# Optimization experiments

Hardware: AMD Instinct MI355X
Metric: run time of the kernel (lower is better)

## Reference

```python
import jax, jax.numpy as jnp
import numpy as np

SEF = 64   # skipped edge features (MLPGraphNetwork default sef)
SNF = 64   # skipped node features (MLPGraphNetwork default snf)
NR_STEPS = 3


def mlp2(x, W0, b0, W1, b1):
    # MyMLP with multI=1.0, relu hidden, linear last, no layernorm
    return jax.nn.relu(x @ W0 + b0) @ W1 + b1


def setup_inputs() -> dict:
    N, E = 50000, 800000
    nrNodeF, nrEdgeF, nrEmbed, nrTypes = 32, 3, 16, 2
    key = jax.random.key(0)
    ks = jax.random.split(key, 20)

    def w(k, fi, fo):
        # torch.normal(0,1) * (2.0 / fan_in)  (relu init in MyMLP)
        return jax.random.normal(k, (fi, fo), jnp.float32) * (2.0 / fi)

    z = lambda n: jnp.zeros((n,), jnp.float32)
    return {
        "edge_index": jax.random.randint(ks[0], (2, E), 0, N),
        "nodeFeatures": jax.random.uniform(ks[1], (N, nrNodeF), jnp.float32),
        "edgeFeatures": jax.random.normal(ks[2], (E, nrEdgeF), jnp.float32),
        "emb": jax.random.normal(ks[3], (nrTypes, nrEmbed), jnp.float32),
        "enc_n_W0": w(ks[4], nrNodeF - 1 + nrEmbed, 128), "enc_n_b0": z(128),
        "enc_n_W1": w(ks[5], 128, 128), "enc_n_b1": z(128),
        "enc_e_W0": w(ks[6], nrEdgeF, 128), "enc_e_b0": z(128),
        "enc_e_W1": w(ks[7], 128, 128), "enc_e_b1": z(128),
        "core_e_W0": w(ks[8], 192, 128), "core_e_b0": z(128),
        "core_e_W1": w(ks[9], 128, 64), "core_e_b1": z(64),
        "core_n_W0": w(ks[10], 128, 128), "core_n_b0": z(128),
        "core_n_W1": w(ks[11], 128, 64), "core_n_b1": z(64),
        "dec_W0": w(ks[12], 128, 128), "dec_b0": z(128),
        "dec_W1": w(ks[13], 128, 3), "dec_b1": z(3),
    }


def reference(edge_index, nodeFeatures, edgeFeatures, emb,
              enc_n_W0, enc_n_b0, enc_n_W1, enc_n_b1,
              enc_e_W0, enc_e_b0, enc_e_W1, enc_e_b1,
              core_e_W0, core_e_b0, core_e_W1, core_e_b1,
              core_n_W0, core_n_b0, core_n_W1, core_n_b1,
              dec_W0, dec_b0, dec_W1, dec_b1):
    N = nodeFeatures.shape[0]
    src, dst = edge_index[0], edge_index[1]  # j (source), i (target)

    # encode: embed particle type from last node feature column
    ptype = (nodeFeatures[:, -1] + 0.5).astype(jnp.int32)
    node = jnp.concatenate([nodeFeatures[:, :-1], emb[ptype]], axis=-1)
    node = mlp2(node, enc_n_W0, enc_n_b0, enc_n_W1, enc_n_b1)          # [N,128]
    edge = mlp2(edgeFeatures, enc_e_W0, enc_e_b0, enc_e_W1, enc_e_b1)  # [E,128]

    ones = jnp.ones((edge_index.shape[1],), node.dtype)
    counts = jnp.maximum(jax.ops.segment_sum(ones, dst, num_segments=N), 1.0)

    # process: shared MLPGraphNetwork applied NR_STEPS times
    for _ in range(NR_STEPS):
        einp = jnp.concatenate([edge[:, SEF:], node[dst][:, SNF:], node[src][:, SNF:]], axis=-1)  # [E,192]
        eout = mlp2(einp, core_e_W0, core_e_b0, core_e_W1, core_e_b1)  # [E,64]
        edge = jnp.concatenate([edge[:, :SEF], edge[:, SEF:] + eout], axis=-1)  # residual tail, [E,128]
        agg = jax.ops.segment_sum(edge, dst, num_segments=N) / counts[:, None]  # mean aggr, [N,128]
        ninp = jnp.concatenate([agg[:, SEF:], node[:, SNF:]], axis=-1)  # [N,128]
        nout = mlp2(ninp, core_n_W0, core_n_b0, core_n_W1, core_n_b1)  # [N,64]
        node = jnp.concatenate([node[:, :SNF], node[:, SNF:] + nout], axis=-1)  # [N,128]

    # decode
    return mlp2(node, dec_W0, dec_b0, dec_W1, dec_b1)  # [N,3]
```

## Files before the change

kernel.cpp:

```cpp
#include <hip/hip_runtime.h>
#include <cstdint>
#include <cstddef>


__global__ void k_zero(int* __restrict__ p, int n) {
    int i = blockIdx.x * 256 + threadIdx.x;
    if (i < n) p[i] = 0;
}


__global__ void k_hist(const int* __restrict__ dst, int* __restrict__ counts, int E) {
    int e = blockIdx.x * 256 + threadIdx.x;
    if (e < E) atomicAdd(&counts[dst[e]], 1);
}

__global__ __launch_bounds__(1024) void k_scan(
    const int* __restrict__ counts, int* __restrict__ row_off,
    int* __restrict__ cursor, float* __restrict__ inv_cnt, int N) {
    __shared__ int wsum[16];
    int t = threadIdx.x;
    int wave = t >> 6, lane = t & 63;
    int carry = 0;
    for (int base = 0; base < N; base += 1024) {
        int i = base + t;
        int v = (i < N) ? counts[i] : 0;
        int s = v;
        #pragma unroll
        for (int off = 1; off < 64; off <<= 1) {
            int u = __shfl_up(s, off, 64);
            if (lane >= off) s += u;
        }
        if (lane == 63) wsum[wave] = s;
        __syncthreads();
        int wpre = 0, full = 0;
        #pragma unroll
        for (int wv = 0; wv < 16; wv++) {
            int x = wsum[wv];
            full += x;
            if (wv < wave) wpre += x;
        }
        if (i < N) {
            int excl = carry + wpre + s - v;
            row_off[i] = excl;
            cursor[i]  = excl;
            inv_cnt[i] = 1.0f / (float)((v > 0) ? v : 1);
        }
        carry += full;
        __syncthreads();
    }
    if (t == 0) row_off[N] = carry;
}

__global__ void k_fill(const int* __restrict__ dst, int* __restrict__ cursor,
                       int* __restrict__ edge_list, int E) {
    int e = blockIdx.x * 256 + threadIdx.x;
    if (e < E) {
        int pos = atomicAdd(&cursor[dst[e]], 1);
        edge_list[pos] = e;
    }
}

__global__ void k_perm_idx(const int* __restrict__ elist,
                           const int* __restrict__ src, const int* __restrict__ dst,
                           int* __restrict__ src_p, int* __restrict__ dst_p, int E) {
    int i = blockIdx.x * 256 + threadIdx.x;
    if (i < E) {
        int e = elist[i];
        src_p[i] = src[e];
        dst_p[i] = dst[e];
    }
}


__global__ void k_embW(const float* __restrict__ emb, const float* __restrict__ W0,
                       const float* __restrict__ b0, float* __restrict__ embW) {
    int c = threadIdx.x;
    #pragma unroll
    for (int p = 0; p < 2; p++) {
        float acc = b0[c];
        #pragma unroll
        for (int k = 0; k < 16; k++)
            acc = fmaf(emb[p * 16 + k], W0[(31 + k) * 128 + c], acc);
        embW[p * 128 + c] = acc;
    }
}


__device__ __forceinline__ void g1_accum32(
    const float4* __restrict__ a4, int kk4,
    const float* __restrict__ W, int cbase, float* __restrict__ h) {
    #pragma clang loop unroll(disable)
    for (int kk = 0; kk < kk4; kk++) {
        float4 a = a4[kk];
        const float* wr = W + (size_t)kk * 4 * 128 + cbase;
        const float4* w0 = reinterpret_cast<const float4*>(wr);
        const float4* w1 = reinterpret_cast<const float4*>(wr + 128);
        const float4* w2 = reinterpret_cast<const float4*>(wr + 256);
        const float4* w3 = reinterpret_cast<const float4*>(wr + 384);
        #pragma unroll
        for (int cg = 0; cg < 8; cg++) {
            float4 p = w0[cg], q = w1[cg], r = w2[cg], s = w3[cg];
            h[cg*4+0] = fmaf(a.w, s.x, fmaf(a.z, r.x, fmaf(a.y, q.x, fmaf(a.x, p.x, h[cg*4+0]))));
            h[cg*4+1] = fmaf(a.w, s.y, fmaf(a.z, r.y, fmaf(a.y, q.y, fmaf(a.x, p.y, h[cg*4+1]))));
            h[cg*4+2] = fmaf(a.w, s.z, fmaf(a.z, r.z, fmaf(a.y, q.z, fmaf(a.x, p.z, h[cg*4+2]))));
            h[cg*4+3] = fmaf(a.w, s.w, fmaf(a.z, r.w, fmaf(a.y, q.w, fmaf(a.x, p.w, h[cg*4+3]))));
        }
    }
}

__device__ __forceinline__ void g1_tail3(
    float x, float y, float z, const float* __restrict__ W, int cbase,
    float* __restrict__ h) {
    const float4* w0 = reinterpret_cast<const float4*>(W + cbase);
    const float4* w1 = reinterpret_cast<const float4*>(W + 128 + cbase);
    const float4* w2 = reinterpret_cast<const float4*>(W + 256 + cbase);
    #pragma unroll
    for (int cg = 0; cg < 8; cg++) {
        float4 p = w0[cg], q = w1[cg], r = w2[cg];
        h[cg*4+0] = fmaf(z, r.x, fmaf(y, q.x, fmaf(x, p.x, h[cg*4+0])));
        h[cg*4+1] = fmaf(z, r.y, fmaf(y, q.y, fmaf(x, p.y, h[cg*4+1])));
        h[cg*4+2] = fmaf(z, r.z, fmaf(y, q.z, fmaf(x, p.z, h[cg*4+2])));
        h[cg*4+3] = fmaf(z, r.w, fmaf(y, q.w, fmaf(x, p.w, h[cg*4+3])));
    }
}

__device__ __forceinline__ void g2_accum64(
    float* __restrict__ sb, const float* __restrict__ hc,
    const float* __restrict__ W1, int kbase, int rs, float* __restrict__ o) {
    int t = threadIdx.x;
    #pragma unroll
    for (int k = 0; k < 32; k++) sb[k * 256 + t] = hc[k];
    __syncthreads();
    #pragma clang loop unroll(disable)
    for (int k = 0; k < 32; k++) {
        float hk = sb[k * 256 + t];
        const float4* w = reinterpret_cast<const float4*>(W1 + (size_t)(kbase + k) * rs);
        #pragma unroll
        for (int cg = 0; cg < 16; cg++) {
            float4 wv = w[cg];
            o[cg*4+0] = fmaf(hk, wv.x, o[cg*4+0]);
            o[cg*4+1] = fmaf(hk, wv.y, o[cg*4+1]);
            o[cg*4+2] = fmaf(hk, wv.z, o[cg*4+2]);
            o[cg*4+3] = fmaf(hk, wv.w, o[cg*4+3]);
        }
    }
    __syncthreads();
}


__global__ __launch_bounds__(256, 2) void k_enc_node_tail(
    const float* __restrict__ nodeF, const float* __restrict__ embW,
    const float* __restrict__ W0, const float* __restrict__ W1,
    const float* __restrict__ b1, float* __restrict__ nodeT, int N) {
    __shared__ float sb[32 * 256];
    int n = blockIdx.x * 256 + threadIdx.x;
    bool valid = n < N;
    int nc = valid ? n : N - 1;
    const float4* nf4 = reinterpret_cast<const float4*>(nodeF + (size_t)nc * 32);
    float4 v7 = nf4[7];
    int p = (int)(v7.w + 0.5f);
    const float4* ew = reinterpret_cast<const float4*>(embW + p * 128);

    float o[64];
    const float4* bv = reinterpret_cast<const float4*>(b1 + 64);
    #pragma unroll
    for (int i = 0; i < 16; i++) {
        float4 b = bv[i];
        o[4*i+0] = b.x; o[4*i+1] = b.y; o[4*i+2] = b.z; o[4*i+3] = b.w;
    }
    #pragma unroll
    for (int ch = 0; ch < 4; ch++) {
        int cbase = ch * 32;
        float h[32];
        #pragma unroll
        for (int i = 0; i < 8; i++) {
            float4 u = ew[ch*8 + i];
            h[4*i+0] = u.x; h[4*i+1] = u.y; h[4*i+2] = u.z; h[4*i+3] = u.w;
        }
        g1_accum32(nf4, 7, W0, cbase, h);
        g1_tail3(v7.x, v7.y, v7.z, W0 + 28*128, cbase, h);
        #pragma unroll
        for (int i = 0; i < 32; i++) h[i] = fmaxf(h[i], 0.0f);
        g2_accum64(sb, h, W1 + 64, cbase, 128, o);
    }
    if (valid) {
        float4* out4 = reinterpret_cast<float4*>(nodeT + (size_t)n * 64);
        #pragma unroll
        for (int i = 0; i < 16; i++)
            out4[i] = make_float4(o[4*i], o[4*i+1], o[4*i+2], o[4*i+3]);
    }
}


__global__ __launch_bounds__(256, 3) void k_enc_edge_T(
    const float* __restrict__ edgeF, const int* __restrict__ perm, int usePerm,
    const float* __restrict__ W0, const float* __restrict__ b0,
    const float* __restrict__ W1, const float* __restrict__ b1,
    float* __restrict__ edgeT, int E) {
    __shared__ float H[128 * 65];
    __shared__ float Wbuf[32 * 68];
    __shared__ float Xs[64 * 4];

    int t = threadIdx.x;
    int base = blockIdx.x * 64;

    if (t < 192) {
        int i = t / 3, j = t - i * 3;
        int e = base + i; int ec = (e < E) ? e : E - 1;
        int e2 = usePerm ? perm[ec] : ec;
        Xs[i * 4 + j] = edgeF[(size_t)e2 * 3 + j];
    }
    __syncthreads();

    int eg = t & 15, cg = t >> 4;
    float c1[4][8];
    {
        float4 b0a = *reinterpret_cast<const float4*>(b0 + cg * 8);
        float4 b0b = *reinterpret_cast<const float4*>(b0 + cg * 8 + 4);
        float bb[8] = {b0a.x,b0a.y,b0a.z,b0a.w,b0b.x,b0b.y,b0b.z,b0b.w};
        #pragma unroll
        for (int ie = 0; ie < 4; ie++)
            #pragma unroll
            for (int jc = 0; jc < 8; jc++) c1[ie][jc] = bb[jc];
    }
    #pragma unroll
    for (int k = 0; k < 3; k++) {
        float4 wa = *reinterpret_cast<const float4*>(W0 + k * 128 + cg * 8);
        float4 wb = *reinterpret_cast<const float4*>(W0 + k * 128 + cg * 8 + 4);
        float ww[8] = {wa.x,wa.y,wa.z,wa.w,wb.x,wb.y,wb.z,wb.w};
        #pragma unroll
        for (int ie = 0; ie < 4; ie++) {
            float a = Xs[(eg + 16 * ie) * 4 + k];
            #pragma unroll
            for (int jc = 0; jc < 8; jc++)
                c1[ie][jc] = fmaf(a, ww[jc], c1[ie][jc]);
        }
    }

    int wr_r = t >> 3, wr_cb = t & 7;
    float4 wreg2[2];
    {
        const float4* wr = reinterpret_cast<const float4*>(
            W1 + (size_t)(wr_r) * 128 + 64 + wr_cb * 8);
        wreg2[0] = wr[0]; wreg2[1] = wr[1];
    }

    #pragma unroll
    for (int ie = 0; ie < 4; ie++)
        #pragma unroll
        for (int jc = 0; jc < 8; jc++)
            H[(cg * 8 + jc) * 65 + eg + 16 * ie] = fmaxf(c1[ie][jc], 0.0f);

    int eg2 = t & 15, cg2 = t >> 4;
    float c2[4][4];
    {
        float4 bv = *reinterpret_cast<const float4*>(b1 + 64 + cg2 * 4);
        #pragma unroll
        for (int ie = 0; ie < 4; ie++) {
            c2[ie][0]=bv.x; c2[ie][1]=bv.y; c2[ie][2]=bv.z; c2[ie][3]=bv.w;
        }
    }
    #pragma clang loop unroll(disable)
    for (int phase = 0; phase < 4; phase++) {
        __syncthreads();
        {
            float* wd = Wbuf + wr_r * 68 + wr_cb * 8;
            wd[0]=wreg2[0].x; wd[1]=wreg2[0].y; wd[2]=wreg2[0].z; wd[3]=wreg2[0].w;
            wd[4]=wreg2[1].x; wd[5]=wreg2[1].y; wd[6]=wreg2[1].z; wd[7]=wreg2[1].w;
        }
        __syncthreads();
        if (phase < 3) {
            const float4* wr = reinterpret_cast<const float4*>(
                W1 + (size_t)((phase + 1) * 32 + wr_r) * 128 + 64 + wr_cb * 8);
            wreg2[0] = wr[0]; wreg2[1] = wr[1];
        }
        #pragma clang loop unroll_count(4)
        for (int k = 0; k < 32; k++) {
            int c = phase * 32 + k;
            float a0 = H[c*65 + eg2*4 + 0];
            float a1 = H[c*65 + eg2*4 + 1];
            float a2 = H[c*65 + eg2*4 + 2];
            float a3 = H[c*65 + eg2*4 + 3];
            float4 b4 = *reinterpret_cast<const float4*>(Wbuf + k * 68 + cg2 * 4);
            float bb[4] = {b4.x, b4.y, b4.z, b4.w};
            #pragma unroll
            for (int jc = 0; jc < 4; jc++) {
                c2[0][jc] = fmaf(a0, bb[jc], c2[0][jc]);
                c2[1][jc] = fmaf(a1, bb[jc], c2[1][jc]);
                c2[2][jc] = fmaf(a2, bb[jc], c2[2][jc]);
                c2[3][jc] = fmaf(a3, bb[jc], c2[3][jc]);
            }
        }
    }
    #pragma unroll
    for (int ie = 0; ie < 4; ie++) {
        int e = base + eg2 * 4 + ie;
        if (e < E) {
            *reinterpret_cast<float4*>(edgeT + (size_t)e * 64 + cg2 * 4) =
                make_float4(c2[ie][0], c2[ie][1], c2[ie][2], c2[ie][3]);
        }
    }
}


__global__ __launch_bounds__(256, 4) void k_node_pre_d(
    const float* __restrict__ nodeT, const float* __restrict__ W0,
    const float* __restrict__ b0, float* __restrict__ Pd, int N) {
    int n = blockIdx.x * 256 + threadIdx.x;
    bool valid = n < N;
    int nc = valid ? n : N - 1;
    const float4* a4 = reinterpret_cast<const float4*>(nodeT + (size_t)nc * 64);

    #pragma unroll
    for (int ch = 0; ch < 4; ch++) {
        int cbase = ch * 32;
        float h[32];
        const float4* b0v = reinterpret_cast<const float4*>(b0 + cbase);
        #pragma unroll
        for (int i = 0; i < 8; i++) {
            float4 b = b0v[i];
            h[4*i+0] = b.x; h[4*i+1] = b.y; h[4*i+2] = b.z; h[4*i+3] = b.w;
        }
        g1_accum32(a4, 16, W0 + 64*128, cbase, h);
        if (valid) {
            float4* o4 = reinterpret_cast<float4*>(Pd + (size_t)n * 128 + cbase);
            #pragma unroll
            for (int i = 0; i < 8; i++)
                o4[i] = make_float4(h[4*i], h[4*i+1], h[4*i+2], h[4*i+3]);
        }
    }
}


__global__ __launch_bounds__(256, 3) void k_edge_core_T(
    float* __restrict__ edgeT, const float* __restrict__ Pd,
    const float* __restrict__ nodeT,
    const int* __restrict__ srcI, const int* __restrict__ dstI,
    const float* __restrict__ W0, const float* __restrict__ W1,
    const float* __restrict__ b1, int E) {
    __shared__ float Abuf[2 * 64 * 65];
    __shared__ float Wbuf[32 * 132];

    int t = threadIdx.x;
    int base = blockIdx.x * 64;

    {
        int i = t >> 2, q = t & 3;
        int e = base + i; int ec = (e < E) ? e : E - 1;
        const float4* er = reinterpret_cast<const float4*>(edgeT + (size_t)ec * 64 + q * 16);
        int s = srcI[ec];
        const float4* sr = reinterpret_cast<const float4*>(nodeT + (size_t)s * 64 + q * 16);
        float* ae = Abuf + i * 65 + q * 16;
        float* as = Abuf + 64 * 65 + i * 65 + q * 16;
        #pragma unroll
        for (int j4 = 0; j4 < 4; j4++) {
            float4 v = er[j4];
            ae[j4*4+0]=v.x; ae[j4*4+1]=v.y; ae[j4*4+2]=v.z; ae[j4*4+3]=v.w;
            float4 w = sr[j4];
            as[j4*4+0]=w.x; as[j4*4+1]=w.y; as[j4*4+2]=w.z; as[j4*4+3]=w.w;
        }
    }

    int eg = t & 15, cg = t >> 4;
    float c1[4][8];
    #pragma unroll
    for (int ie = 0; ie < 4; ie++) {
        int e = base + eg + 16 * ie; int ec = (e < E) ? e : E - 1;
        int d = dstI[ec];
        const float4* pr = reinterpret_cast<const float4*>(Pd + (size_t)d * 128 + cg * 8);
        float4 p0 = pr[0], p1 = pr[1];
        c1[ie][0]=p0.x; c1[ie][1]=p0.y; c1[ie][2]=p0.z; c1[ie][3]=p0.w;
        c1[ie][4]=p1.x; c1[ie][5]=p1.y; c1[ie][6]=p1.z; c1[ie][7]=p1.w;
    }

    int wr_r = t >> 3, wr_cb = t & 7;
    float4 wreg[4];
    {
        const float4* wr = reinterpret_cast<const float4*>(
            W0 + (size_t)(0 + wr_r) * 128 + wr_cb * 16);
        wreg[0]=wr[0]; wreg[1]=wr[1]; wreg[2]=wr[2]; wreg[3]=wr[3];
    }
    #pragma clang loop unroll(disable)
    for (int phase = 0; phase < 4; phase++) {
        const float* Asrc = Abuf + ((phase < 2) ? 0 : 64 * 65);
        int koff = (phase & 1) * 32;
        __syncthreads();
        {
            float* wd = Wbuf + wr_r * 132 + wr_cb * 16;
            #pragma unroll
            for (int j4 = 0; j4 < 4; j4++) {
                wd[j4*4+0]=wreg[j4].x; wd[j4*4+1]=wreg[j4].y;
                wd[j4*4+2]=wreg[j4].z; wd[j4*4+3]=wreg[j4].w;
            }
        }
        __syncthreads();
        if (phase < 3) {
            int wrow_n = (phase + 1 < 2) ? (phase + 1) * 32 : 128 + (phase - 1) * 32;
            const float4* wr = reinterpret_cast<const float4*>(
                W0 + (size_t)(wrow_n + wr_r) * 128 + wr_cb * 16);
            wreg[0]=wr[0]; wreg[1]=wr[1]; wreg[2]=wr[2]; wreg[3]=wr[3];
        }
        #pragma clang loop unroll_count(4)
        for (int k = 0; k < 32; k++) {
            float a0 = Asrc[(eg + 16*0)*65 + koff + k];
            float a1 = Asrc[(eg + 16*1)*65 + koff + k];
            float a2 = Asrc[(eg + 16*2)*65 + koff + k];
            float a3 = Asrc[(eg + 16*3)*65 + koff + k];
            const float* wrp = Wbuf + k * 132 + cg * 8;
            float4 bq0 = *reinterpret_cast<const float4*>(wrp);
            float4 bq1 = *reinterpret_cast<const float4*>(wrp + 4);
            float bb[8] = {bq0.x,bq0.y,bq0.z,bq0.w,bq1.x,bq1.y,bq1.z,bq1.w};
            #pragma unroll
            for (int jc = 0; jc < 8; jc++) {
                c1[0][jc] = fmaf(a0, bb[jc], c1[0][jc]);
                c1[1][jc] = fmaf(a1, bb[jc], c1[1][jc]);
                c1[2][jc] = fmaf(a2, bb[jc], c1[2][jc]);
                c1[3][jc] = fmaf(a3, bb[jc], c1[3][jc]);
            }
        }
    }

    float4 wreg2[2];
    {
        const float4* wr = reinterpret_cast<const float4*>(
            W1 + (size_t)(wr_r) * 64 + wr_cb * 8);
        wreg2[0] = wr[0]; wreg2[1] = wr[1];
    }

    __syncthreads();
    float* H = Abuf;
    #pragma unroll
    for (int ie = 0; ie < 4; ie++)
        #pragma unroll
        for (int jc = 0; jc < 8; jc++)
            H[(cg*8 + jc) * 65 + eg + 16*ie] = fmaxf(c1[ie][jc], 0.0f);

    int eg2 = t & 15, cg2 = t >> 4;
    float c2[4][4];
    {
        float4 bv = *reinterpret_cast<const float4*>(b1 + cg2 * 4);
        #pragma unroll
        for (int ie = 0; ie < 4; ie++) {
            c2[ie][0]=bv.x; c2[ie][1]=bv.y; c2[ie][2]=bv.z; c2[ie][3]=bv.w;
        }
    }
    #pragma clang loop unroll(disable)
    for (int phase = 0; phase < 4; phase++) {
        __syncthreads();
        {
            float* wd = Wbuf + wr_r * 68 + wr_cb * 8;
            wd[0]=wreg2[0].x; wd[1]=wreg2[0].y; wd[2]=wreg2[0].z; wd[3]=wreg2[0].w;
            wd[4]=wreg2[1].x; wd[5]=wreg2[1].y; wd[6]=wreg2[1].z; wd[7]=wreg2[1].w;
        }
        __syncthreads();
        if (phase < 3) {
            const float4* wr = reinterpret_cast<const float4*>(
                W1 + (size_t)((phase + 1) * 32 + wr_r) * 64 + wr_cb * 8);
            wreg2[0] = wr[0]; wreg2[1] = wr[1];
        }
        #pragma clang loop unroll_count(4)
        for (int k = 0; k < 32; k++) {
            int c = phase * 32 + k;
            float a0 = H[c*65 + eg2*4 + 0];
            float a1 = H[c*65 + eg2*4 + 1];
            float a2 = H[c*65 + eg2*4 + 2];
            float a3 = H[c*65 + eg2*4 + 3];
            float4 b4 = *reinterpret_cast<const float4*>(Wbuf + k * 68 + cg2 * 4);
            float bb[4] = {b4.x, b4.y, b4.z, b4.w};
            #pragma unroll
            for (int jc = 0; jc < 4; jc++) {
                c2[0][jc] = fmaf(a0, bb[jc], c2[0][jc]);
                c2[1][jc] = fmaf(a1, bb[jc], c2[1][jc]);
                c2[2][jc] = fmaf(a2, bb[jc], c2[2][jc]);
                c2[3][jc] = fmaf(a3, bb[jc], c2[3][jc]);
            }
        }
    }

    #pragma unroll
    for (int ie = 0; ie < 4; ie++) {
        int e = base + eg2 * 4 + ie;
        if (e < E) {
            float4* er = reinterpret_cast<float4*>(edgeT + (size_t)e * 64 + cg2 * 4);
            float4 old = *er;
            old.x += c2[ie][0]; old.y += c2[ie][1];
            old.z += c2[ie][2]; old.w += c2[ie][3];
            *er = old;
        }
    }
}


__global__ __launch_bounds__(256, 3) void k_node_core_T(
    const float* __restrict__ aggT, float* __restrict__ nodeT,
    const float* __restrict__ W0, const float* __restrict__ b0,
    const float* __restrict__ W1, const float* __restrict__ b1, int N) {
    __shared__ float Abuf[64 * 132];
    __shared__ float Wbuf[32 * 132];

    int t = threadIdx.x;
    int base = blockIdx.x * 64;

    {
        int i = t >> 2, q = t & 3;
        int n = base + i; int nc = (n < N) ? n : N - 1;
        const float4* gr = reinterpret_cast<const float4*>(aggT + (size_t)nc * 64 + q * 16);
        const float4* tr = reinterpret_cast<const float4*>(nodeT + (size_t)nc * 64 + q * 16);
        float* ag = Abuf + i * 132 + q * 16;
        float* at = Abuf + i * 132 + 64 + q * 16;
        #pragma unroll
        for (int j4 = 0; j4 < 4; j4++) {
            float4 v = gr[j4];
            ag[j4*4+0]=v.x; ag[j4*4+1]=v.y; ag[j4*4+2]=v.z; ag[j4*4+3]=v.w;
            float4 w = tr[j4];
            at[j4*4+0]=w.x; at[j4*4+1]=w.y; at[j4*4+2]=w.z; at[j4*4+3]=w.w;
        }
    }

    int ng = t & 15, cg = t >> 4;
    float c1[4][8];
    {
        float4 b0a = *reinterpret_cast<const float4*>(b0 + cg * 8);
        float4 b0b = *reinterpret_cast<const float4*>(b0 + cg * 8 + 4);
        float bb[8] = {b0a.x,b0a.y,b0a.z,b0a.w,b0b.x,b0b.y,b0b.z,b0b.w};
        #pragma unroll
        for (int in = 0; in < 4; in++)
            #pragma unroll
            for (int jc = 0; jc < 8; jc++) c1[in][jc] = bb[jc];
    }

    int wr_r = t >> 3, wr_cb = t & 7;
    float4 wreg[4];
    {
        const float4* wr = reinterpret_cast<const float4*>(
            W0 + (size_t)(wr_r) * 128 + wr_cb * 16);
        wreg[0]=wr[0]; wreg[1]=wr[1]; wreg[2]=wr[2]; wreg[3]=wr[3];
    }
    #pragma clang loop unroll(disable)
    for (int phase = 0; phase < 4; phase++) {
        int koff = phase * 32;
        __syncthreads();
        {
            float* wd = Wbuf + wr_r * 132 + wr_cb * 16;
            #pragma unroll
            for (int j4 = 0; j4 < 4; j4++) {
                wd[j4*4+0]=wreg[j4].x; wd[j4*4+1]=wreg[j4].y;
                wd[j4*4+2]=wreg[j4].z; wd[j4*4+3]=wreg[j4].w;
            }
        }
        __syncthreads();
        if (phase < 3) {
            const float4* wr = reinterpret_cast<const float4*>(
                W0 + (size_t)((phase + 1) * 32 + wr_r) * 128 + wr_cb * 16);
            wreg[0]=wr[0]; wreg[1]=wr[1]; wreg[2]=wr[2]; wreg[3]=wr[3];
        }
        #pragma clang loop unroll_count(4)
        for (int k = 0; k < 32; k++) {
            float a0 = Abuf[(ng + 16*0)*132 + koff + k];
            float a1 = Abuf[(ng + 16*1)*132 + koff + k];
            float a2 = Abuf[(ng + 16*2)*132 + koff + k];
            float a3 = Abuf[(ng + 16*3)*132 + koff + k];
            const float* wrp = Wbuf + k * 132 + cg * 8;
            float4 bq0 = *reinterpret_cast<const float4*>(wrp);
            float4 bq1 = *reinterpret_cast<const float4*>(wrp + 4);
            float bb[8] = {bq0.x,bq0.y,bq0.z,bq0.w,bq1.x,bq1.y,bq1.z,bq1.w};
            #pragma unroll
            for (int jc = 0; jc < 8; jc++) {
                c1[0][jc] = fmaf(a0, bb[jc], c1[0][jc]);
                c1[1][jc] = fmaf(a1, bb[jc], c1[1][jc]);
                c1[2][jc] = fmaf(a2, bb[jc], c1[2][jc]);
                c1[3][jc] = fmaf(a3, bb[jc], c1[3][jc]);
            }
        }
    }

    float4 wreg2[2];
    {
        const float4* wr = reinterpret_cast<const float4*>(
            W1 + (size_t)(wr_r) * 64 + wr_cb * 8);
        wreg2[0] = wr[0]; wreg2[1] = wr[1];
    }

    __syncthreads();
    float* H = Abuf;
    #pragma unroll
    for (int in = 0; in < 4; in++)
        #pragma unroll
        for (int jc = 0; jc < 8; jc++)
            H[(cg*8 + jc) * 65 + ng + 16*in] = fmaxf(c1[in][jc], 0.0f);

    int ng2 = t & 15, cg2 = t >> 4;
    float c2[4][4];
    {
        float4 bv = *reinterpret_cast<const float4*>(b1 + cg2 * 4);
        #pragma unroll
        for (int in = 0; in < 4; in++) {
            c2[in][0]=bv.x; c2[in][1]=bv.y; c2[in][2]=bv.z; c2[in][3]=bv.w;
        }
    }
    #pragma clang loop unroll(disable)
    for (int phase = 0; phase < 4; phase++) {
        __syncthreads();
        {
            float* wd = Wbuf + wr_r * 68 + wr_cb * 8;
            wd[0]=wreg2[0].x; wd[1]=wreg2[0].y; wd[2]=wreg2[0].z; wd[3]=wreg2[0].w;
            wd[4]=wreg2[1].x; wd[5]=wreg2[1].y; wd[6]=wreg2[1].z; wd[7]=wreg2[1].w;
        }
        __syncthreads();
        if (phase < 3) {
            const float4* wr = reinterpret_cast<const float4*>(
                W1 + (size_t)((phase + 1) * 32 + wr_r) * 64 + wr_cb * 8);
            wreg2[0] = wr[0]; wreg2[1] = wr[1];
        }
        #pragma clang loop unroll_count(4)
        for (int k = 0; k < 32; k++) {
            int c = phase * 32 + k;
            float a0 = H[c*65 + ng2*4 + 0];
            float a1 = H[c*65 + ng2*4 + 1];
            float a2 = H[c*65 + ng2*4 + 2];
            float a3 = H[c*65 + ng2*4 + 3];
            float4 b4 = *reinterpret_cast<const float4*>(Wbuf + k * 68 + cg2 * 4);
            float bb[4] = {b4.x, b4.y, b4.z, b4.w};
            #pragma unroll
            for (int jc = 0; jc < 4; jc++) {
                c2[0][jc] = fmaf(a0, bb[jc], c2[0][jc]);
                c2[1][jc] = fmaf(a1, bb[jc], c2[1][jc]);
                c2[2][jc] = fmaf(a2, bb[jc], c2[2][jc]);
                c2[3][jc] = fmaf(a3, bb[jc], c2[3][jc]);
            }
        }
    }

    #pragma unroll
    for (int in = 0; in < 4; in++) {
        int n = base + ng2 * 4 + in;
        if (n < N) {
            float4* nr = reinterpret_cast<float4*>(nodeT + (size_t)n * 64 + cg2 * 4);
            float4 old = *nr;
            old.x += c2[in][0]; old.y += c2[in][1];
            old.z += c2[in][2]; old.w += c2[in][3];
            *nr = old;
        }
    }
}


__global__ __launch_bounds__(256, 2) void k_edge_core_B(
    float* __restrict__ edgeT, const float* __restrict__ nodeT,
    const int* __restrict__ src, const int* __restrict__ dst,
    const float* __restrict__ W0, const float* __restrict__ b0,
    const float* __restrict__ W1, const float* __restrict__ b1, int E) {
    __shared__ float sb[32 * 256];
    int e = blockIdx.x * 256 + threadIdx.x;
    bool valid = e < E;
    int ec = valid ? e : E - 1;
    int d = dst[ec], s = src[ec];
    const float4* a4 = reinterpret_cast<const float4*>(edgeT + (size_t)ec * 64);
    const float4* d4 = reinterpret_cast<const float4*>(nodeT + (size_t)d * 64);
    const float4* s4 = reinterpret_cast<const float4*>(nodeT + (size_t)s * 64);

    float o[64];
    const float4* bv = reinterpret_cast<const float4*>(b1);
    #pragma unroll
    for (int i = 0; i < 16; i++) {
        float4 b = bv[i];
        o[4*i+0] = b.x; o[4*i+1] = b.y; o[4*i+2] = b.z; o[4*i+3] = b.w;
    }
    #pragma unroll
    for (int ch = 0; ch < 4; ch++) {
        int cbase = ch * 32;
        float h[32];
        const float4* b0v = reinterpret_cast<const float4*>(b0 + cbase);
        #pragma unroll
        for (int i = 0; i < 8; i++) {
            float4 b = b0v[i];
            h[4*i+0] = b.x; h[4*i+1] = b.y; h[4*i+2] = b.z; h[4*i+3] = b.w;
        }
        g1_accum32(a4, 16, W0, cbase, h);
        g1_accum32(d4, 16, W0 + 64*128, cbase, h);
        g1_accum32(s4, 16, W0 + 128*128, cbase, h);
        #pragma unroll
        for (int i = 0; i < 32; i++) h[i] = fmaxf(h[i], 0.0f);
        g2_accum64(sb, h, W1, cbase, 64, o);
    }
    if (valid) {
        float4* eo4 = reinterpret_cast<float4*>(edgeT + (size_t)e * 64);
        #pragma unroll
        for (int i = 0; i < 16; i++) {
            float4 t = a4[i];
            t.x += o[4*i+0]; t.y += o[4*i+1];
            t.z += o[4*i+2]; t.w += o[4*i+3];
            eo4[i] = t;
        }
    }
}


__global__ __launch_bounds__(256) void k_agg_csr(
    const float* __restrict__ edgeT, const int* __restrict__ row_off,
    const float* __restrict__ inv_cnt, float* __restrict__ aggT, int N) {
    int n = blockIdx.x * 4 + (threadIdx.x >> 6);
    int lane = threadIdx.x & 63;
    if (n >= N) return;
    int beg = row_off[n], end = row_off[n + 1];
    double s = 0.0;
    for (int idx = beg; idx < end; idx++)
        s += (double)edgeT[(size_t)idx * 64 + lane];
    aggT[(size_t)n * 64 + lane] = (float)(s * (double)inv_cnt[n]);
}

__global__ __launch_bounds__(256) void k_agg_gather(
    const float* __restrict__ edgeT, const int* __restrict__ row_off,
    const int* __restrict__ edge_list, const float* __restrict__ inv_cnt,
    float* __restrict__ aggT, int N) {
    int n = blockIdx.x * 4 + (threadIdx.x >> 6);
    int lane = threadIdx.x & 63;
    if (n >= N) return;
    int beg = row_off[n], end = row_off[n + 1];
    double s = 0.0;
    for (int idx = beg; idx < end; idx++) {
        int e = edge_list[idx];
        s += (double)edgeT[(size_t)e * 64 + lane];
    }
    aggT[(size_t)n * 64 + lane] = (float)(s * (double)inv_cnt[n]);
}


__global__ __launch_bounds__(256, 2) void k_decode(
    const float* __restrict__ nodeF, const float* __restrict__ embW,
    const float* __restrict__ encW0, const float* __restrict__ encW1,
    const float* __restrict__ encb1, const float* __restrict__ nodeT,
    const float* __restrict__ W0, const float* __restrict__ b0,
    const float* __restrict__ W1, const float* __restrict__ b1,
    float* __restrict__ out, int N) {
    __shared__ float sb[64 * 256];
    int t = threadIdx.x;
    int n = blockIdx.x * 256 + t;
    bool valid = n < N;
    int nc = valid ? n : N - 1;
    const float4* nf4 = reinterpret_cast<const float4*>(nodeF + (size_t)nc * 32);
    const float4* t4  = reinterpret_cast<const float4*>(nodeT + (size_t)nc * 64);
    float4 v7 = nf4[7];
    int p = (int)(v7.w + 0.5f);
    const float4* ew = reinterpret_cast<const float4*>(embW + p * 128);

    float head[64];
    const float4* ebv = reinterpret_cast<const float4*>(encb1);
    #pragma unroll
    for (int i = 0; i < 16; i++) {
        float4 b = ebv[i];
        head[4*i+0] = b.x; head[4*i+1] = b.y; head[4*i+2] = b.z; head[4*i+3] = b.w;
    }
    #pragma unroll
    for (int ch = 0; ch < 4; ch++) {
        int cbase = ch * 32;
        float h[32];
        #pragma unroll
        for (int i = 0; i < 8; i++) {
            float4 u = ew[ch*8 + i];
            h[4*i+0] = u.x; h[4*i+1] = u.y; h[4*i+2] = u.z; h[4*i+3] = u.w;
        }
        g1_accum32(nf4, 7, encW0, cbase, h);
        g1_tail3(v7.x, v7.y, v7.z, encW0 + 28*128, cbase, h);
        #pragma unroll
        for (int i = 0; i < 32; i++) h[i] = fmaxf(h[i], 0.0f);
        g2_accum64(sb, h, encW1, cbase, 128, head);
    }

    #pragma unroll
    for (int k = 0; k < 64; k++) sb[k * 256 + t] = head[k];
    __syncthreads();

    float h2[128];
    #pragma unroll
    for (int ch = 0; ch < 4; ch++) {
        int cbase = ch * 32;
        float* hc = &h2[ch * 32];
        const float4* b0v = reinterpret_cast<const float4*>(b0 + cbase);
        #pragma unroll
        for (int i = 0; i < 8; i++) {
            float4 b = b0v[i];
            hc[4*i+0] = b.x; hc[4*i+1] = b.y; hc[4*i+2] = b.z; hc[4*i+3] = b.w;
        }
        #pragma clang loop unroll(disable)
        for (int k = 0; k < 64; k++) {
            float hk = sb[k * 256 + t];
            const float4* w = reinterpret_cast<const float4*>(W0 + (size_t)k * 128 + cbase);
            #pragma unroll
            for (int cg = 0; cg < 8; cg++) {
                float4 wv = w[cg];
                hc[cg*4+0] = fmaf(hk, wv.x, hc[cg*4+0]);
                hc[cg*4+1] = fmaf(hk, wv.y, hc[cg*4+1]);
                hc[cg*4+2] = fmaf(hk, wv.z, hc[cg*4+2]);
                hc[cg*4+3] = fmaf(hk, wv.w, hc[cg*4+3]);
            }
        }
        g1_accum32(t4, 16, W0 + 64*128, cbase, hc);
    }
    __syncthreads();

    float o0 = b1[0], o1 = b1[1], o2 = b1[2];
    #pragma unroll
    for (int ch = 0; ch < 4; ch++) {
        int kb = ch * 32;
        #pragma unroll
        for (int k = 0; k < 32; k++) sb[k * 256 + t] = fmaxf(h2[kb + k], 0.0f);
        __syncthreads();
        #pragma clang loop unroll(disable)
        for (int k = 0; k < 32; k++) {
            float hk = sb[k * 256 + t];
            const float* w = W1 + (size_t)(kb + k) * 3;
            o0 = fmaf(hk, w[0], o0);
            o1 = fmaf(hk, w[1], o1);
            o2 = fmaf(hk, w[2], o2);
        }
        __syncthreads();
    }
    if (valid) {
        out[(size_t)n * 3 + 0] = o0;
        out[(size_t)n * 3 + 1] = o1;
        out[(size_t)n * 3 + 2] = o2;
    }
}


extern "C" void kernel_launch(void* const* d_in, const int* in_sizes, int n_in,
                              void* d_out, int out_size, void* d_ws, size_t ws_size,
                              hipStream_t stream) {
    const int*   edge_index = (const int*)  d_in[0];
    const float* nodeF      = (const float*)d_in[1];
    const float* edgeF      = (const float*)d_in[2];
    const float* emb        = (const float*)d_in[3];
    const float* enc_n_W0   = (const float*)d_in[4];
    const float* enc_n_b0   = (const float*)d_in[5];
    const float* enc_n_W1   = (const float*)d_in[6];
    const float* enc_n_b1   = (const float*)d_in[7];
    const float* enc_e_W0   = (const float*)d_in[8];
    const float* enc_e_b0   = (const float*)d_in[9];
    const float* enc_e_W1   = (const float*)d_in[10];
    const float* enc_e_b1   = (const float*)d_in[11];
    const float* core_e_W0  = (const float*)d_in[12];
    const float* core_e_b0  = (const float*)d_in[13];
    const float* core_e_W1  = (const float*)d_in[14];
    const float* core_e_b1  = (const float*)d_in[15];
    const float* core_n_W0  = (const float*)d_in[16];
    const float* core_n_b0  = (const float*)d_in[17];
    const float* core_n_W1  = (const float*)d_in[18];
    const float* core_n_b1  = (const float*)d_in[19];
    const float* dec_W0     = (const float*)d_in[20];
    const float* dec_b0     = (const float*)d_in[21];
    const float* dec_W1     = (const float*)d_in[22];
    const float* dec_b1     = (const float*)d_in[23];
    (void)n_in; (void)out_size;

    const int E = in_sizes[0] / 2;
    const int N = in_sizes[1] / 32;
    const int* src = edge_index;
    const int* dst = edge_index + E;

    auto al = [](size_t x) { return (x + 255) & ~(size_t)255; };
    const size_t szEdgeT = al((size_t)E * 64 * 4);
    const size_t szNodeT = al((size_t)N * 64 * 4);
    const size_t szP     = al((size_t)N * 128 * 4);
    const size_t szAgg   = al((size_t)N * 64 * 4);
    const size_t szElist = al((size_t)E * 4);
    const size_t szN4    = al((size_t)N * 4);
    const size_t szRow   = al((size_t)(N + 1) * 4);
    const size_t szEmbW  = al(2 * 128 * 4);
    const size_t base = szEdgeT + szNodeT + szElist + szRow + 3 * szN4 + szEmbW;
    const size_t needCSR = base + 2 * szElist + szP;
    const size_t needAp  = base + szP;
    const int plan = (ws_size >= needCSR) ? 0 : (ws_size >= needAp) ? 1 : 2;

    char* ws = (char*)d_ws;
    size_t off = 0;
    auto carve = [&](size_t bytes) -> char* { char* p = ws + off; off += bytes; return p; };
    float* edgeT   = (float*)carve(szEdgeT);
    float* nodeT   = (float*)carve(szNodeT);
    int*   elist   = (int*)  carve(szElist);
    int*   row_off = (int*)  carve(szRow);
    int*   counts  = (int*)  carve(szN4);
    int*   cursor  = (int*)  carve(szN4);
    float* inv_cnt = (float*)carve(szN4);
    float* embW    = (float*)carve(szEmbW);
    int *src_p = nullptr, *dst_p = nullptr;
    float *Pd = nullptr, *aggT = nullptr;
    if (plan == 0) {
        src_p = (int*)carve(szElist);
        dst_p = (int*)carve(szElist);
        Pd = (float*)carve(szP); aggT = Pd;
    } else if (plan == 1) {
        Pd = (float*)carve(szP); aggT = Pd;
    } else {
        aggT = (float*)carve(szAgg);
    }

    int blkE = (E + 255) / 256;
    int blkN = (N + 255) / 256;
    int blkT = (E + 63) / 64;
    int blkNT = (N + 63) / 64;

    k_zero<<<(N + 255) / 256, 256, 0, stream>>>(counts, N);
    k_hist<<<blkE, 256, 0, stream>>>(dst, counts, E);
    k_scan<<<1, 1024, 0, stream>>>(counts, row_off, cursor, inv_cnt, N);
    k_fill<<<blkE, 256, 0, stream>>>(dst, cursor, elist, E);
    if (plan == 0)
        k_perm_idx<<<blkE, 256, 0, stream>>>(elist, src, dst, src_p, dst_p, E);

    k_embW<<<1, 128, 0, stream>>>(emb, enc_n_W0, enc_n_b0, embW);
    k_enc_node_tail<<<blkN, 256, 0, stream>>>(nodeF, embW, enc_n_W0, enc_n_W1,
                                              enc_n_b1, nodeT, N);
    k_enc_edge_T<<<blkT, 256, 0, stream>>>(edgeF, elist, (plan == 0) ? 1 : 0,
                                           enc_e_W0, enc_e_b0, enc_e_W1, enc_e_b1,
                                           edgeT, E);

    for (int step = 0; step < 3; step++) {
        if (plan == 0) {
            k_node_pre_d<<<blkN, 256, 0, stream>>>(nodeT, core_e_W0, core_e_b0, Pd, N);
            k_edge_core_T<<<blkT, 256, 0, stream>>>(edgeT, Pd, nodeT, src_p, dst_p,
                                                    core_e_W0, core_e_W1, core_e_b1, E);
            k_agg_csr<<<(N + 3) / 4, 256, 0, stream>>>(edgeT, row_off, inv_cnt, aggT, N);
        } else if (plan == 1) {
            k_node_pre_d<<<blkN, 256, 0, stream>>>(nodeT, core_e_W0, core_e_b0, Pd, N);
            k_edge_core_T<<<blkT, 256, 0, stream>>>(edgeT, Pd, nodeT, src, dst,
                                                    core_e_W0, core_e_W1, core_e_b1, E);
            k_agg_gather<<<(N + 3) / 4, 256, 0, stream>>>(edgeT, row_off, elist,
                                                          inv_cnt, aggT, N);
        } else {
            k_edge_core_B<<<blkE, 256, 0, stream>>>(edgeT, nodeT, src, dst,
                                                    core_e_W0, core_e_b0,
                                                    core_e_W1, core_e_b1, E);
            k_agg_gather<<<(N + 3) / 4, 256, 0, stream>>>(edgeT, row_off, elist,
                                                          inv_cnt, aggT, N);
        }
        k_node_core_T<<<blkNT, 256, 0, stream>>>(aggT, nodeT, core_n_W0, core_n_b0,
                                                 core_n_W1, core_n_b1, N);
    }
    k_decode<<<blkN, 256, 0, stream>>>(nodeF, embW, enc_n_W0, enc_n_W1, enc_n_b1,
                                       nodeT, dec_W0, dec_b0, dec_W1, dec_b1,
                                       (float*)d_out, N);
}
```

Before: 2.859 ms.

## Tile node precompute through shared memory and vectorize LDS accesses with padding 68

Replaces the one-thread-per-node node precompute (each thread streaming all weights from global) with a 64-node tiled kernel that stages node rows and 32-row weight slabs in shared memory and computes a 4x8 register tile per thread. Shared buffers across the edge, encoder and node kernels are re-padded from stride 65 to 68 so the hidden-activation reads and the staging stores become float4 LDS operations. This cuts the number of LDS instructions and the global weight traffic, at the cost of extra shared memory and possibly more bank conflicts on the strided scalar column reads.

```diff
diff --git a/kernel.cpp b/kernel.cpp
--- a/kernel.cpp
+++ b/kernel.cpp
@@ -197,7 +197,7 @@
     const float* __restrict__ W0, const float* __restrict__ b0,
     const float* __restrict__ W1, const float* __restrict__ b1,
     float* __restrict__ edgeT, int E) {
-    __shared__ float H[128 * 65];
+    __shared__ float H[128 * 68];
     __shared__ float Wbuf[32 * 68];
     __shared__ float Xs[64 * 4];
 
@@ -249,7 +249,7 @@
     for (int ie = 0; ie < 4; ie++)
         #pragma unroll
         for (int jc = 0; jc < 8; jc++)
-            H[(cg * 8 + jc) * 65 + eg + 16 * ie] = fmaxf(c1[ie][jc], 0.0f);
+            H[(cg * 8 + jc) * 68 + eg + 16 * ie] = fmaxf(c1[ie][jc], 0.0f);
 
     int eg2 = t & 15, cg2 = t >> 4;
     float c2[4][4];
@@ -277,18 +277,16 @@
         #pragma clang loop unroll_count(4)
         for (int k = 0; k < 32; k++) {
             int c = phase * 32 + k;
-            float a0 = H[c*65 + eg2*4 + 0];
-            float a1 = H[c*65 + eg2*4 + 1];
-            float a2 = H[c*65 + eg2*4 + 2];
-            float a3 = H[c*65 + eg2*4 + 3];
+            float4 av = *reinterpret_cast<const float4*>(H + c * 68 + eg2 * 4);
             float4 b4 = *reinterpret_cast<const float4*>(Wbuf + k * 68 + cg2 * 4);
             float bb[4] = {b4.x, b4.y, b4.z, b4.w};
+            float aa[4] = {av.x, av.y, av.z, av.w};
             #pragma unroll
             for (int jc = 0; jc < 4; jc++) {
-                c2[0][jc] = fmaf(a0, bb[jc], c2[0][jc]);
-                c2[1][jc] = fmaf(a1, bb[jc], c2[1][jc]);
-                c2[2][jc] = fmaf(a2, bb[jc], c2[2][jc]);
-                c2[3][jc] = fmaf(a3, bb[jc], c2[3][jc]);
+                c2[0][jc] = fmaf(aa[0], bb[jc], c2[0][jc]);
+                c2[1][jc] = fmaf(aa[1], bb[jc], c2[1][jc]);
+                c2[2][jc] = fmaf(aa[2], bb[jc], c2[2][jc]);
+                c2[3][jc] = fmaf(aa[3], bb[jc], c2[3][jc]);
             }
         }
     }
@@ -303,30 +301,74 @@
 }
 
 
-__global__ __launch_bounds__(256, 4) void k_node_pre_d(
+__global__ __launch_bounds__(256, 4) void k_node_pre_T(
     const float* __restrict__ nodeT, const float* __restrict__ W0,
     const float* __restrict__ b0, float* __restrict__ Pd, int N) {
-    int n = blockIdx.x * 256 + threadIdx.x;
-    bool valid = n < N;
-    int nc = valid ? n : N - 1;
-    const float4* a4 = reinterpret_cast<const float4*>(nodeT + (size_t)nc * 64);
-
-    #pragma unroll
-    for (int ch = 0; ch < 4; ch++) {
-        int cbase = ch * 32;
-        float h[32];
-        const float4* b0v = reinterpret_cast<const float4*>(b0 + cbase);
-        #pragma unroll
-        for (int i = 0; i < 8; i++) {
-            float4 b = b0v[i];
-            h[4*i+0] = b.x; h[4*i+1] = b.y; h[4*i+2] = b.z; h[4*i+3] = b.w;
-        }
-        g1_accum32(a4, 16, W0 + 64*128, cbase, h);
-        if (valid) {
-            float4* o4 = reinterpret_cast<float4*>(Pd + (size_t)n * 128 + cbase);
-            #pragma unroll
-            for (int i = 0; i < 8; i++)
-                o4[i] = make_float4(h[4*i], h[4*i+1], h[4*i+2], h[4*i+3]);
+    __shared__ float As[64 * 68];
+    __shared__ float Wbuf[32 * 132];
+
+    int t = threadIdx.x;
+    int base = blockIdx.x * 64;
+
+    {
+        int i = t >> 2, q = t & 3;
+        int n = base + i; int nc = (n < N) ? n : N - 1;
+        const float4* tr = reinterpret_cast<const float4*>(nodeT + (size_t)nc * 64 + q * 16);
+        float4* ad = reinterpret_cast<float4*>(As + i * 68 + q * 16);
+        ad[0]=tr[0]; ad[1]=tr[1]; ad[2]=tr[2]; ad[3]=tr[3];
+    }
+
+    int ng = t & 15, cg = t >> 4;
+    float c[4][8];
+    {
+        float4 b0a = *reinterpret_cast<const float4*>(b0 + cg * 8);
+        float4 b0b = *reinterpret_cast<const float4*>(b0 + cg * 8 + 4);
+        float bb[8] = {b0a.x,b0a.y,b0a.z,b0a.w,b0b.x,b0b.y,b0b.z,b0b.w};
+        #pragma unroll
+        for (int in = 0; in < 4; in++)
+            #pragma unroll
+            for (int jc = 0; jc < 8; jc++) c[in][jc] = bb[jc];
+    }
+
+    int wr_r = t >> 3, wr_cb = t & 7;
+    #pragma clang loop unroll(disable)
+    for (int phase = 0; phase < 2; phase++) {
+        __syncthreads();
+        {
+            const float4* wr = reinterpret_cast<const float4*>(
+                W0 + (size_t)(64 + phase * 32 + wr_r) * 128 + wr_cb * 16);
+            float4* wd = reinterpret_cast<float4*>(Wbuf + wr_r * 132 + wr_cb * 16);
+            wd[0]=wr[0]; wd[1]=wr[1]; wd[2]=wr[2]; wd[3]=wr[3];
+        }
+        __syncthreads();
+        int koff = phase * 32;
+        #pragma clang loop unroll_count(4)
+        for (int k = 0; k < 32; k++) {
+            float a0 = As[(ng + 16*0)*68 + koff + k];
+            float a1 = As[(ng + 16*1)*68 + koff + k];
+            float a2 = As[(ng + 16*2)*68 + koff + k];
+            float a3 = As[(ng + 16*3)*68 + koff + k];
+            const float* wrp = Wbuf + k * 132 + cg * 8;
+            float4 bq0 = *reinterpret_cast<const float4*>(wrp);
+            float4 bq1 = *reinterpret_cast<const float4*>(wrp + 4);
+            float bb[8] = {bq0.x,bq0.y,bq0.z,bq0.w,bq1.x,bq1.y,bq1.z,bq1.w};
+            #pragma unroll
+            for (int jc = 0; jc < 8; jc++) {
+                c[0][jc] = fmaf(a0, bb[jc], c[0][jc]);
+                c[1][jc] = fmaf(a1, bb[jc], c[1][jc]);
+                c[2][jc] = fmaf(a2, bb[jc], c[2][jc]);
+                c[3][jc] = fmaf(a3, bb[jc], c[3][jc]);
+            }
+        }
+    }
+
+    #pragma unroll
+    for (int in = 0; in < 4; in++) {
+        int n = base + ng + 16 * in;
+        if (n < N) {
+            float4* o4 = reinterpret_cast<float4*>(Pd + (size_t)n * 128 + cg * 8);
+            o4[0] = make_float4(c[in][0], c[in][1], c[in][2], c[in][3]);
+            o4[1] = make_float4(c[in][4], c[in][5], c[in][6], c[in][7]);
         }
     }
 }
@@ -338,7 +380,7 @@
     const int* __restrict__ srcI, const int* __restrict__ dstI,
     const float* __restrict__ W0, const float* __restrict__ W1,
     const float* __restrict__ b1, int E) {
-    __shared__ float Abuf[2 * 64 * 65];
+    __shared__ float Abuf[2 * 64 * 68];
     __shared__ float Wbuf[32 * 132];
 
     int t = threadIdx.x;
@@ -350,15 +392,10 @@
         const float4* er = reinterpret_cast<const float4*>(edgeT + (size_t)ec * 64 + q * 16);
         int s = srcI[ec];
         const float4* sr = reinterpret_cast<const float4*>(nodeT + (size_t)s * 64 + q * 16);
-        float* ae = Abuf + i * 65 + q * 16;
-        float* as = Abuf + 64 * 65 + i * 65 + q * 16;
-        #pragma unroll
-        for (int j4 = 0; j4 < 4; j4++) {
-            float4 v = er[j4];
-            ae[j4*4+0]=v.x; ae[j4*4+1]=v.y; ae[j4*4+2]=v.z; ae[j4*4+3]=v.w;
-            float4 w = sr[j4];
-            as[j4*4+0]=w.x; as[j4*4+1]=w.y; as[j4*4+2]=w.z; as[j4*4+3]=w.w;
-        }
+        float4* ae = reinterpret_cast<float4*>(Abuf + i * 68 + q * 16);
+        float4* as = reinterpret_cast<float4*>(Abuf + 64 * 68 + i * 68 + q * 16);
+        #pragma unroll
+        for (int j4 = 0; j4 < 4; j4++) { ae[j4] = er[j4]; as[j4] = sr[j4]; }
     }
 
     int eg = t & 15, cg = t >> 4;
@@ -377,21 +414,17 @@
     float4 wreg[4];
     {
         const float4* wr = reinterpret_cast<const float4*>(
-            W0 + (size_t)(0 + wr_r) * 128 + wr_cb * 16);
+            W0 + (size_t)wr_r * 128 + wr_cb * 16);
         wreg[0]=wr[0]; wreg[1]=wr[1]; wreg[2]=wr[2]; wreg[3]=wr[3];
     }
     #pragma clang loop unroll(disable)
     for (int phase = 0; phase < 4; phase++) {
-        const float* Asrc = Abuf + ((phase < 2) ? 0 : 64 * 65);
+        const float* Asrc = Abuf + ((phase < 2) ? 0 : 64 * 68);
         int koff = (phase & 1) * 32;
         __syncthreads();
         {
-            float* wd = Wbuf + wr_r * 132 + wr_cb * 16;
-            #pragma unroll
-            for (int j4 = 0; j4 < 4; j4++) {
-                wd[j4*4+0]=wreg[j4].x; wd[j4*4+1]=wreg[j4].y;
-                wd[j4*4+2]=wreg[j4].z; wd[j4*4+3]=wreg[j4].w;
-            }
+            float4* wd = reinterpret_cast<float4*>(Wbuf + wr_r * 132 + wr_cb * 16);
+            wd[0]=wreg[0]; wd[1]=wreg[1]; wd[2]=wreg[2]; wd[3]=wreg[3];
         }
         __syncthreads();
         if (phase < 3) {
@@ -402,10 +435,10 @@
         }
         #pragma clang loop unroll_count(4)
         for (int k = 0; k < 32; k++) {
-            float a0 = Asrc[(eg + 16*0)*65 + koff + k];
-            float a1 = Asrc[(eg + 16*1)*65 + koff + k];
-            float a2 = Asrc[(eg + 16*2)*65 + koff + k];
-            float a3 = Asrc[(eg + 16*3)*65 + koff + k];
+            float a0 = Asrc[(eg + 16*0)*68 + koff + k];
+            float a1 = Asrc[(eg + 16*1)*68 + koff + k];
+            float a2 = Asrc[(eg + 16*2)*68 + koff + k];
+            float a3 = Asrc[(eg + 16*3)*68 + koff + k];
             const float* wrp = Wbuf + k * 132 + cg * 8;
             float4 bq0 = *reinterpret_cast<const float4*>(wrp);
             float4 bq1 = *reinterpret_cast<const float4*>(wrp + 4);
@@ -433,7 +466,7 @@
     for (int ie = 0; ie < 4; ie++)
         #pragma unroll
         for (int jc = 0; jc < 8; jc++)
-            H[(cg*8 + jc) * 65 + eg + 16*ie] = fmaxf(c1[ie][jc], 0.0f);
+            H[(cg*8 + jc) * 68 + eg + 16*ie] = fmaxf(c1[ie][jc], 0.0f);
 
     int eg2 = t & 15, cg2 = t >> 4;
     float c2[4][4];
@@ -461,18 +494,16 @@
         #pragma clang loop unroll_count(4)
         for (int k = 0; k < 32; k++) {
             int c = phase * 32 + k;
-            float a0 = H[c*65 + eg2*4 + 0];
-            float a1 = H[c*65 + eg2*4 + 1];
-            float a2 = H[c*65 + eg2*4 + 2];
-            float a3 = H[c*65 + eg2*4 + 3];
+            float4 av = *reinterpret_cast<const float4*>(H + c * 68 + eg2 * 4);
             float4 b4 = *reinterpret_cast<const float4*>(Wbuf + k * 68 + cg2 * 4);
             float bb[4] = {b4.x, b4.y, b4.z, b4.w};
+            float aa[4] = {av.x, av.y, av.z, av.w};
             #pragma unroll
             for (int jc = 0; jc < 4; jc++) {
-                c2[0][jc] = fmaf(a0, bb[jc], c2[0][jc]);
-                c2[1][jc] = fmaf(a1, bb[jc], c2[1][jc]);
-                c2[2][jc] = fmaf(a2, bb[jc], c2[2][jc]);
-                c2[3][jc] = fmaf(a3, bb[jc], c2[3][jc]);
+                c2[0][jc] = fmaf(aa[0], bb[jc], c2[0][jc]);
+                c2[1][jc] = fmaf(aa[1], bb[jc], c2[1][jc]);
+                c2[2][jc] = fmaf(aa[2], bb[jc], c2[2][jc]);
+                c2[3][jc] = fmaf(aa[3], bb[jc], c2[3][jc]);
             }
         }
     }
@@ -495,7 +526,7 @@
     const float* __restrict__ aggT, float* __restrict__ nodeT,
     const float* __restrict__ W0, const float* __restrict__ b0,
     const float* __restrict__ W1, const float* __restrict__ b1, int N) {
-    __shared__ float Abuf[64 * 132];
+    __shared__ float Abuf[64 * 136];
     __shared__ float Wbuf[32 * 132];
 
     int t = threadIdx.x;
@@ -506,15 +537,10 @@
         int n = base + i; int nc = (n < N) ? n : N - 1;
         const float4* gr = reinterpret_cast<const float4*>(aggT + (size_t)nc * 64 + q * 16);
         const float4* tr = reinterpret_cast<const float4*>(nodeT + (size_t)nc * 64 + q * 16);
-        float* ag = Abuf + i * 132 + q * 16;
-        float* at = Abuf + i * 132 + 64 + q * 16;
-        #pragma unroll
-        for (int j4 = 0; j4 < 4; j4++) {
-            float4 v = gr[j4];
-            ag[j4*4+0]=v.x; ag[j4*4+1]=v.y; ag[j4*4+2]=v.z; ag[j4*4+3]=v.w;
-            float4 w = tr[j4];
-            at[j4*4+0]=w.x; at[j4*4+1]=w.y; at[j4*4+2]=w.z; at[j4*4+3]=w.w;
-        }
+        float4* ag = reinterpret_cast<float4*>(Abuf + i * 132 + q * 16);
+        float4* at = reinterpret_cast<float4*>(Abuf + i * 132 + 64 + q * 16);
+        #pragma unroll
+        for (int j4 = 0; j4 < 4; j4++) { ag[j4] = gr[j4]; at[j4] = tr[j4]; }
     }
 
     int ng = t & 15, cg = t >> 4;
@@ -533,7 +559,7 @@
     float4 wreg[4];
     {
         const float4* wr = reinterpret_cast<const float4*>(
-            W0 + (size_t)(wr_r) * 128 + wr_cb * 16);
+            W0 + (size_t)wr_r * 128 + wr_cb * 16);
         wreg[0]=wr[0]; wreg[1]=wr[1]; wreg[2]=wr[2]; wreg[3]=wr[3];
     }
     #pragma clang loop unroll(disable)
@@ -541,12 +567,8 @@
         int koff = phase * 32;
         __syncthreads();
         {
-            float* wd = Wbuf + wr_r * 132 + wr_cb * 16;
-            #pragma unroll
-            for (int j4 = 0; j4 < 4; j4++) {
-                wd[j4*4+0]=wreg[j4].x; wd[j4*4+1]=wreg[j4].y;
-                wd[j4*4+2]=wreg[j4].z; wd[j4*4+3]=wreg[j4].w;
-            }
+            float4* wd = reinterpret_cast<float4*>(Wbuf + wr_r * 132 + wr_cb * 16);
+            wd[0]=wreg[0]; wd[1]=wreg[1]; wd[2]=wreg[2]; wd[3]=wreg[3];
         }
         __syncthreads();
         if (phase < 3) {
@@ -577,7 +599,7 @@
     float4 wreg2[2];
     {
         const float4* wr = reinterpret_cast<const float4*>(
-            W1 + (size_t)(wr_r) * 64 + wr_cb * 8);
+            W1 + (size_t)wr_r * 64 + wr_cb * 8);
         wreg2[0] = wr[0]; wreg2[1] = wr[1];
     }
 
@@ -587,7 +609,7 @@
     for (int in = 0; in < 4; in++)
         #pragma unroll
         for (int jc = 0; jc < 8; jc++)
-            H[(cg*8 + jc) * 65 + ng + 16*in] = fmaxf(c1[in][jc], 0.0f);
+            H[(cg*8 + jc) * 68 + ng + 16*in] = fmaxf(c1[in][jc], 0.0f);
 
     int ng2 = t & 15, cg2 = t >> 4;
     float c2[4][4];
@@ -615,18 +637,16 @@
         #pragma clang loop unroll_count(4)
         for (int k = 0; k < 32; k++) {
             int c = phase * 32 + k;
-            float a0 = H[c*65 + ng2*4 + 0];
-            float a1 = H[c*65 + ng2*4 + 1];
-            float a2 = H[c*65 + ng2*4 + 2];
-            float a3 = H[c*65 + ng2*4 + 3];
+            float4 av = *reinterpret_cast<const float4*>(H + c * 68 + ng2 * 4);
             float4 b4 = *reinterpret_cast<const float4*>(Wbuf + k * 68 + cg2 * 4);
             float bb[4] = {b4.x, b4.y, b4.z, b4.w};
+            float aa[4] = {av.x, av.y, av.z, av.w};
             #pragma unroll
             for (int jc = 0; jc < 4; jc++) {
-                c2[0][jc] = fmaf(a0, bb[jc], c2[0][jc]);
-                c2[1][jc] = fmaf(a1, bb[jc], c2[1][jc]);
-                c2[2][jc] = fmaf(a2, bb[jc], c2[2][jc]);
-                c2[3][jc] = fmaf(a3, bb[jc], c2[3][jc]);
+                c2[0][jc] = fmaf(aa[0], bb[jc], c2[0][jc]);
+                c2[1][jc] = fmaf(aa[1], bb[jc], c2[1][jc]);
+                c2[2][jc] = fmaf(aa[2], bb[jc], c2[2][jc]);
+                c2[3][jc] = fmaf(aa[3], bb[jc], c2[3][jc]);
             }
         }
     }
@@ -916,12 +936,12 @@
 
     for (int step = 0; step < 3; step++) {
         if (plan == 0) {
-            k_node_pre_d<<<blkN, 256, 0, stream>>>(nodeT, core_e_W0, core_e_b0, Pd, N);
+            k_node_pre_T<<<blkNT, 256, 0, stream>>>(nodeT, core_e_W0, core_e_b0, Pd, N);
             k_edge_core_T<<<blkT, 256, 0, stream>>>(edgeT, Pd, nodeT, src_p, dst_p,
                                                     core_e_W0, core_e_W1, core_e_b1, E);
             k_agg_csr<<<(N + 3) / 4, 256, 0, stream>>>(edgeT, row_off, inv_cnt, aggT, N);
         } else if (plan == 1) {
-            k_node_pre_d<<<blkN, 256, 0, stream>>>(nodeT, core_e_W0, core_e_b0, Pd, N);
+            k_node_pre_T<<<blkNT, 256, 0, stream>>>(nodeT, core_e_W0, core_e_b0, Pd, N);
             k_edge_core_T<<<blkT, 256, 0, stream>>>(edgeT, Pd, nodeT, src, dst,
                                                     core_e_W0, core_e_W1, core_e_b1, E);
             k_agg_gather<<<(N + 3) / 4, 256, 0, stream>>>(edgeT, row_off, elist,
```

Measured after the change: 2.720 ms. 1.05x faster.
